# Performance work log

Measured on AMD Instinct MI355X. Metric: run time of the kernel, lower is better.

## Reference

```python
import jax, jax.numpy as jnp
import numpy as np

N_NODES = 2000
N_EDGES = 32000
B, T = 16, 20
OUT = 8      # GAT out_feats (num_heads=1)
HID = 24     # LSTM hidden
FC_OUT = 160  # num_airports * prediction_horizon = 20*8
FCC_OUT = 20
NEG_SLOPE = 0.2


def setup_inputs() -> dict:
    key = jax.random.key(0)
    ks = jax.random.split(key, 20)
    s = 0.1
    return {
        "x": jax.random.normal(ks[0], (B, T, N_NODES, 1), jnp.float32),
        "edge_w": jax.random.uniform(ks[1], (B, T, N_EDGES, 1), jnp.float32),
        "src": jax.random.randint(ks[2], (N_EDGES,), 0, N_NODES, dtype=jnp.int32),
        "dst": jax.random.randint(ks[3], (N_EDGES,), 0, N_NODES, dtype=jnp.int32),
        # EdgeGATConv params
        "W_node": jax.random.normal(ks[4], (1, OUT), jnp.float32) * s,
        "W_edge": jax.random.normal(ks[5], (1, OUT), jnp.float32) * s,
        "attn_l": jax.random.normal(ks[6], (OUT,), jnp.float32) * s,
        "attn_e": jax.random.normal(ks[7], (OUT,), jnp.float32) * s,
        "attn_r": jax.random.normal(ks[8], (OUT,), jnp.float32) * s,
        "gat_b": jnp.zeros((OUT,), jnp.float32),
        # LSTM params (PyTorch gate order i,f,g,o)
        "w_ih": jax.random.normal(ks[9], (4 * HID, OUT), jnp.float32) * s,
        "w_hh": jax.random.normal(ks[10], (4 * HID, HID), jnp.float32) * s,
        "b_ih": jnp.zeros((4 * HID,), jnp.float32),
        "b_hh": jnp.zeros((4 * HID,), jnp.float32),
        # fc / fcc
        "fc_w": jax.random.normal(ks[11], (FC_OUT, HID), jnp.float32) * s,
        "fc_b": jnp.zeros((FC_OUT,), jnp.float32),
        "fcc_w": jax.random.normal(ks[12], (FCC_OUT, 8 * 20), jnp.float32) * s,
        "fcc_b": jnp.zeros((FCC_OUT,), jnp.float32),
    }


def _gat_graph(xg, wg, src, dst, W_node, W_edge, attn_l, attn_e, attn_r, gat_b):
    # xg: [N,1], wg: [E,1] -> pooled graph feature [OUT]
    fs = xg @ W_node                      # [N,OUT] projected node feats
    fe = wg @ W_edge                      # [E,OUT] projected edge feats
    el = fs @ attn_l                      # [N]
    er = fs @ attn_r                      # [N]  (dst == src features, homogeneous graph)
    ee = fe @ attn_e                      # [E]
    e = jax.nn.leaky_relu(el[src] + ee + er[dst], NEG_SLOPE)  # [E]
    # edge_softmax over incoming edges of each dst node
    emax = jax.ops.segment_max(e, dst, num_segments=N_NODES)  # [N]
    num = jnp.exp(e - emax[dst])
    den = jax.ops.segment_sum(num, dst, num_segments=N_NODES)
    a = num / den[dst]                    # [E]
    msg = a[:, None] * (fs[src] + fe)     # [E,OUT]
    rst = jax.ops.segment_sum(msg, dst, num_segments=N_NODES) + gat_b  # [N,OUT]
    return rst.mean(axis=0)               # graph mean-pool -> [OUT]


def reference(x, edge_w, src, dst, W_node, W_edge, attn_l, attn_e, attn_r, gat_b,
              w_ih, w_hh, b_ih, b_hh, fc_w, fc_b, fcc_w, fcc_b):
    # GAT per (series, time) graph, vmapped over flattened B*T axis
    xf = x.reshape(B * T, N_NODES, 1)
    wf = edge_w.reshape(B * T, N_EDGES, 1)
    gat = jax.vmap(lambda xg, wg: _gat_graph(xg, wg, src, dst, W_node, W_edge,
                                             attn_l, attn_e, attn_r, gat_b))
    feats = gat(xf, wf).reshape(B, T, OUT)  # [B,T,8]
    # Dropout(0.1) -> identity in eval mode

    # LSTM (batch_first), zero initial state
    def step(carry, xt):
        h, c = carry
        g = xt @ w_ih.T + h @ w_hh.T + b_ih + b_hh  # [B,4H]
        i, f, gg, o = jnp.split(g, 4, axis=-1)
        c = jax.nn.sigmoid(f) * c + jax.nn.sigmoid(i) * jnp.tanh(gg)
        h = jax.nn.sigmoid(o) * jnp.tanh(c)
        return (h, c), h

    h0 = jnp.zeros((B, HID), feats.dtype)
    (_, _), hs = jax.lax.scan(step, (h0, h0), jnp.swapaxes(feats, 0, 1))
    outputs = jnp.swapaxes(hs, 0, 1)      # [B,T,24]; squeeze(0) is a no-op for B>1

    out = outputs @ fc_w.T + fc_b         # [B,T,160]
    out = out.reshape(-1, 8 * 20) @ fcc_w.T + fcc_b  # [B*T,20]
    return out
```

## Files before the change

kernel.cpp:

```cpp
#include <hip/hip_runtime.h>
#include <math.h>

#define N_NODES 2000
#define N_EDGES 32000
#define BB 16
#define TT 20
#define NG (BB*TT)
#define OUTF 8
#define HID 24
#define FC_OUTD 160
#define FCC_OUTD 20

#define SC_DEN 4194304.0f
#define SC_T1  1048576.0f
#define SC_T2  4194304.0f


__global__ __launch_bounds__(1024) void gat_fused(
    const float* __restrict__ x, const float* __restrict__ edge_w,
    const int* __restrict__ src, const int* __restrict__ dst,
    const float* __restrict__ W_node, const float* __restrict__ W_edge,
    const float* __restrict__ attn_l, const float* __restrict__ attn_e,
    const float* __restrict__ attn_r, const float* __restrict__ gat_b,
    float* __restrict__ feats)
{
    __shared__ float xs[N_NODES];
    __shared__ int   aden[N_NODES];
    __shared__ int   at1[N_NODES];
    __shared__ int   at2[N_NODES];
    __shared__ double wr1[16], wr2[16];

    const int g   = blockIdx.x;
    const int tid = threadIdx.x;

    float cl = 0.f, ce = 0.f, cr = 0.f;
#pragma unroll
    for (int k = 0; k < OUTF; ++k) {
        cl += W_node[k] * attn_l[k];
        cr += W_node[k] * attn_r[k];
        ce += W_edge[k] * attn_e[k];
    }

    const float* xg = x + (size_t)g * N_NODES;
    const float* wg = edge_w + (size_t)g * N_EDGES;

    {
        const float4* xg4 = (const float4*)xg;
        for (int i = tid; i < N_NODES/4; i += 1024)
            ((float4*)xs)[i] = xg4[i];
        for (int i = tid; i < N_NODES; i += 1024) {
            aden[i] = 0; at1[i] = 0; at2[i] = 0;
        }
    }
    __syncthreads();

    const int4*   src4 = (const int4*)src;
    const int4*   dst4 = (const int4*)dst;
    const float4* wg4  = (const float4*)wg;
#pragma unroll
    for (int k = 0; k < (N_EDGES/4 + 1023) / 1024; ++k) {
        int c = tid + k * 1024;
        if (c < N_EDGES/4) {
            int4   sv = src4[c];
            int4   dv = dst4[c];
            float4 wv = wg4[c];
#pragma unroll
            for (int j = 0; j < 4; ++j) {
                int   s = (&sv.x)[j];
                int   d = (&dv.x)[j];
                float w = (&wv.x)[j];
                float xsv = xs[s];
                float ev  = cl * xsv + ce * w + cr * xs[d];
                ev = fmaxf(ev, 0.2f * ev);
                float num = __expf(ev);
                atomicAdd(&aden[d], __float2int_rn(num * SC_DEN));
                atomicAdd(&at1[d],  __float2int_rn(num * xsv * SC_T1));
                atomicAdd(&at2[d],  __float2int_rn(num * w * SC_T2));
            }
        }
    }
    __syncthreads();

    double s1 = 0.0, s2 = 0.0;
    for (int n = tid; n < N_NODES; n += 1024) {
        int deni = aden[n];
        if (deni > 0) {
            double inv = 1.0 / (double)deni;
            s1 += (double)at1[n] * 4.0 * inv;
            s2 += (double)at2[n] * inv;
        }
    }
#pragma unroll
    for (int off = 32; off > 0; off >>= 1) {
        s1 += __shfl_down(s1, off, 64);
        s2 += __shfl_down(s2, off, 64);
    }
    int wave = tid >> 6, lane = tid & 63;
    if (lane == 0) { wr1[wave] = s1; wr2[wave] = s2; }
    __syncthreads();
    if (tid == 0) {
        double a = 0.0, c = 0.0;
#pragma unroll
        for (int w = 0; w < 16; ++w) { a += wr1[w]; c += wr2[w]; }
#pragma unroll
        for (int k = 0; k < OUTF; ++k)
            feats[g * OUTF + k] = gat_b[k] +
                (float)((a * (double)W_node[k] + c * (double)W_edge[k]) / (double)N_NODES);
    }
}


__device__ __forceinline__ float fast_sigmoid(float v) {
    return 1.f / (1.f + __expf(-v));
}
__device__ __forceinline__ float fast_tanh(float v) {
    float t = __expf(2.f * v);
    return (t - 1.f) / (t + 1.f);
}

__global__ __launch_bounds__(128) void lstm_head(
    const float* __restrict__ feats,
    const float* __restrict__ w_ih, const float* __restrict__ w_hh,
    const float* __restrict__ b_ih, const float* __restrict__ b_hh,
    const float* __restrict__ fc_w, const float* __restrict__ fc_b,
    const float* __restrict__ fcc_w, const float* __restrict__ fcc_b,
    float* __restrict__ out)
{
    __shared__ float s_fccw[FCC_OUTD * FC_OUTD];
    __shared__ float s_fcw[FC_OUTD * HID];
    __shared__ float s_fcb[FC_OUTD];
    __shared__ float s_M[FCC_OUTD * HID];
    __shared__ float s_b2[FCC_OUTD];
    __shared__ float s_xt[TT * OUTF];
    __shared__ float s_g[96];
    __shared__ float s_h[HID], s_c[HID];
    __shared__ float s_hs[TT * HID];

    const int b   = blockIdx.x;
    const int tid = threadIdx.x;

    for (int i = tid; i < FCC_OUTD * FC_OUTD; i += 128) s_fccw[i] = fcc_w[i];
    for (int i = tid; i < FC_OUTD * HID;      i += 128) s_fcw[i]  = fc_w[i];
    for (int i = tid; i < FC_OUTD;            i += 128) s_fcb[i]  = fc_b[i];
    for (int i = tid; i < TT * OUTF;          i += 128) s_xt[i]   = feats[b * TT * OUTF + i];
    if (tid < HID) { s_h[tid] = 0.f; s_c[tid] = 0.f; }

    float rw_ih[OUTF], rw_hh[HID], rbias = 0.f;
    if (tid < 96) {
        rbias = b_ih[tid] + b_hh[tid];
#pragma unroll
        for (int k = 0; k < OUTF; ++k) rw_ih[k] = w_ih[tid * OUTF + k];
#pragma unroll
        for (int k = 0; k < HID; ++k) rw_hh[k] = w_hh[tid * HID + k];
    }
    __syncthreads();

    for (int u = tid; u < FCC_OUTD * HID; u += 128) {
        int j = u / HID, h = u % HID;
        float acc = 0.f;
        for (int m = 0; m < FC_OUTD; ++m)
            acc += s_fccw[j * FC_OUTD + m] * s_fcw[m * HID + h];
        s_M[u] = acc;
    }
    if (tid < FCC_OUTD) {
        float acc = fcc_b[tid];
        for (int m = 0; m < FC_OUTD; ++m) acc += s_fccw[tid * FC_OUTD + m] * s_fcb[m];
        s_b2[tid] = acc;
    }

    for (int t = 0; t < TT; ++t) {
        if (tid < 96) {
            float acc = rbias;
            const float* xt = &s_xt[t * OUTF];
#pragma unroll
            for (int k = 0; k < OUTF; ++k) acc += xt[k] * rw_ih[k];
#pragma unroll
            for (int k = 0; k < HID; ++k) acc += s_h[k] * rw_hh[k];
            s_g[tid] = acc;
        }
        __syncthreads();
        if (tid < HID) {
            float i_ = fast_sigmoid(s_g[tid]);
            float f_ = fast_sigmoid(s_g[24 + tid]);
            float g_ = fast_tanh(s_g[48 + tid]);
            float o_ = fast_sigmoid(s_g[72 + tid]);
            float c = f_ * s_c[tid] + i_ * g_;
            s_c[tid] = c;
            float h = o_ * fast_tanh(c);
            s_h[tid] = h;
            s_hs[t * HID + tid] = h;
        }
        __syncthreads();
    }

    for (int u = tid; u < TT * FCC_OUTD; u += 128) {
        int t = u / FCC_OUTD, j = u % FCC_OUTD;
        float acc = s_b2[j];
        const float* hr = &s_hs[t * HID];
#pragma unroll
        for (int h = 0; h < HID; ++h) acc += hr[h] * s_M[j * HID + h];
        out[(b * TT + t) * FCC_OUTD + j] = acc;
    }
}

extern "C" void kernel_launch(void* const* d_in, const int* in_sizes, int n_in,
                              void* d_out, int out_size, void* d_ws, size_t ws_size,
                              hipStream_t stream) {
    const float* x      = (const float*)d_in[0];
    const float* edge_w = (const float*)d_in[1];
    const int*   src    = (const int*)d_in[2];
    const int*   dst    = (const int*)d_in[3];
    const float* W_node = (const float*)d_in[4];
    const float* W_edge = (const float*)d_in[5];
    const float* attn_l = (const float*)d_in[6];
    const float* attn_e = (const float*)d_in[7];
    const float* attn_r = (const float*)d_in[8];
    const float* gat_b  = (const float*)d_in[9];
    const float* w_ih   = (const float*)d_in[10];
    const float* w_hh   = (const float*)d_in[11];
    const float* b_ih   = (const float*)d_in[12];
    const float* b_hh   = (const float*)d_in[13];
    const float* fc_w   = (const float*)d_in[14];
    const float* fc_b   = (const float*)d_in[15];
    const float* fcc_w  = (const float*)d_in[16];
    const float* fcc_b  = (const float*)d_in[17];

    float* feats = (float*)d_ws;
    float* out   = (float*)d_out;

    gat_fused<<<NG, 1024, 0, stream>>>(x, edge_w, src, dst, W_node, W_edge,
                                       attn_l, attn_e, attn_r, gat_b, feats);
    lstm_head<<<BB, 128, 0, stream>>>(feats, w_ih, w_hh, b_ih, b_hh,
                                      fc_w, fc_b, fcc_w, fcc_b, out);
}
```

Baseline: 50.56 us.

## Precompute fcc·fc product in extra GAT block and hoist LSTM input projection

Adds an extra block to the GAT launch that computes the folded fcc_w·fc_w matrix and bias once into workspace, running alongside the graph blocks. The LSTM kernel then no longer loads the large fc weights or repeats that fold in each of its 16 blocks. It also precomputes the input-to-gate projection for all timesteps in parallel before the serial recurrence, which shortens each step. The cost is more workspace traffic and one extra block in the GAT grid.

```diff
diff --git a/kernel.cpp b/kernel.cpp
--- a/kernel.cpp
+++ b/kernel.cpp
@@ -16,13 +16,16 @@
 #define SC_T2  4194304.0f
 
 
+
 __global__ __launch_bounds__(1024) void gat_fused(
     const float* __restrict__ x, const float* __restrict__ edge_w,
     const int* __restrict__ src, const int* __restrict__ dst,
     const float* __restrict__ W_node, const float* __restrict__ W_edge,
     const float* __restrict__ attn_l, const float* __restrict__ attn_e,
     const float* __restrict__ attn_r, const float* __restrict__ gat_b,
-    float* __restrict__ feats)
+    const float* __restrict__ fc_w, const float* __restrict__ fc_b,
+    const float* __restrict__ fcc_w, const float* __restrict__ fcc_b,
+    float* __restrict__ ws)
 {
     __shared__ float xs[N_NODES];
     __shared__ int   aden[N_NODES];
@@ -30,8 +33,28 @@
     __shared__ int   at2[N_NODES];
     __shared__ double wr1[16], wr2[16];
 
-    const int g   = blockIdx.x;
     const int tid = threadIdx.x;
+
+    if (blockIdx.x == NG) {
+        if (tid < FCC_OUTD * HID) {
+            int j = tid / HID, h = tid % HID;
+            float acc = 0.f;
+#pragma unroll 4
+            for (int m = 0; m < FC_OUTD; ++m)
+                acc += fcc_w[j * FC_OUTD + m] * fc_w[m * HID + h];
+            ws[NG * OUTF + tid] = acc;
+        } else if (tid < FCC_OUTD * HID + FCC_OUTD) {
+            int j = tid - FCC_OUTD * HID;
+            float acc = fcc_b[j];
+#pragma unroll 4
+            for (int m = 0; m < FC_OUTD; ++m)
+                acc += fcc_w[j * FC_OUTD + m] * fc_b[m];
+            ws[NG * OUTF + FCC_OUTD * HID + j] = acc;
+        }
+        return;
+    }
+
+    const int g = blockIdx.x;
 
     float cl = 0.f, ce = 0.f, cr = 0.f;
 #pragma unroll
@@ -104,7 +127,7 @@
         for (int w = 0; w < 16; ++w) { a += wr1[w]; c += wr2[w]; }
 #pragma unroll
         for (int k = 0; k < OUTF; ++k)
-            feats[g * OUTF + k] = gat_b[k] +
+            ws[g * OUTF + k] = gat_b[k] +
                 (float)((a * (double)W_node[k] + c * (double)W_edge[k]) / (double)N_NODES);
     }
 }
@@ -119,19 +142,16 @@
 }
 
 __global__ __launch_bounds__(128) void lstm_head(
-    const float* __restrict__ feats,
+    const float* __restrict__ ws,
     const float* __restrict__ w_ih, const float* __restrict__ w_hh,
     const float* __restrict__ b_ih, const float* __restrict__ b_hh,
-    const float* __restrict__ fc_w, const float* __restrict__ fc_b,
-    const float* __restrict__ fcc_w, const float* __restrict__ fcc_b,
     float* __restrict__ out)
 {
-    __shared__ float s_fccw[FCC_OUTD * FC_OUTD];
-    __shared__ float s_fcw[FC_OUTD * HID];
-    __shared__ float s_fcb[FC_OUTD];
     __shared__ float s_M[FCC_OUTD * HID];
     __shared__ float s_b2[FCC_OUTD];
     __shared__ float s_xt[TT * OUTF];
+    __shared__ float s_bias[96];
+    __shared__ float s_xg[TT * 96];
     __shared__ float s_g[96];
     __shared__ float s_h[HID], s_c[HID];
     __shared__ float s_hs[TT * HID];
@@ -139,41 +159,32 @@
     const int b   = blockIdx.x;
     const int tid = threadIdx.x;
 
-    for (int i = tid; i < FCC_OUTD * FC_OUTD; i += 128) s_fccw[i] = fcc_w[i];
-    for (int i = tid; i < FC_OUTD * HID;      i += 128) s_fcw[i]  = fc_w[i];
-    for (int i = tid; i < FC_OUTD;            i += 128) s_fcb[i]  = fc_b[i];
-    for (int i = tid; i < TT * OUTF;          i += 128) s_xt[i]   = feats[b * TT * OUTF + i];
+    for (int i = tid; i < FCC_OUTD * HID; i += 128) s_M[i]  = ws[NG * OUTF + i];
+    if (tid < FCC_OUTD) s_b2[tid] = ws[NG * OUTF + FCC_OUTD * HID + tid];
+    for (int i = tid; i < TT * OUTF; i += 128) s_xt[i] = ws[b * TT * OUTF + i];
+    if (tid < 96) s_bias[tid] = b_ih[tid] + b_hh[tid];
     if (tid < HID) { s_h[tid] = 0.f; s_c[tid] = 0.f; }
 
-    float rw_ih[OUTF], rw_hh[HID], rbias = 0.f;
+    float rw_hh[HID];
     if (tid < 96) {
-        rbias = b_ih[tid] + b_hh[tid];
-#pragma unroll
-        for (int k = 0; k < OUTF; ++k) rw_ih[k] = w_ih[tid * OUTF + k];
 #pragma unroll
         for (int k = 0; k < HID; ++k) rw_hh[k] = w_hh[tid * HID + k];
     }
     __syncthreads();
 
-    for (int u = tid; u < FCC_OUTD * HID; u += 128) {
-        int j = u / HID, h = u % HID;
-        float acc = 0.f;
-        for (int m = 0; m < FC_OUTD; ++m)
-            acc += s_fccw[j * FC_OUTD + m] * s_fcw[m * HID + h];
-        s_M[u] = acc;
-    }
-    if (tid < FCC_OUTD) {
-        float acc = fcc_b[tid];
-        for (int m = 0; m < FC_OUTD; ++m) acc += s_fccw[tid * FC_OUTD + m] * s_fcb[m];
-        s_b2[tid] = acc;
-    }
+    for (int u = tid; u < TT * 96; u += 128) {
+        int t = u / 96, j = u % 96;
+        float acc = s_bias[j];
+        const float* xt = &s_xt[t * OUTF];
+#pragma unroll
+        for (int k = 0; k < OUTF; ++k) acc += xt[k] * w_ih[j * OUTF + k];
+        s_xg[u] = acc;
+    }
+    __syncthreads();
 
     for (int t = 0; t < TT; ++t) {
         if (tid < 96) {
-            float acc = rbias;
-            const float* xt = &s_xt[t * OUTF];
-#pragma unroll
-            for (int k = 0; k < OUTF; ++k) acc += xt[k] * rw_ih[k];
+            float acc = s_xg[t * 96 + tid];
 #pragma unroll
             for (int k = 0; k < HID; ++k) acc += s_h[k] * rw_hh[k];
             s_g[tid] = acc;
@@ -225,11 +236,11 @@
     const float* fcc_w  = (const float*)d_in[16];
     const float* fcc_b  = (const float*)d_in[17];
 
-    float* feats = (float*)d_ws;
-    float* out   = (float*)d_out;
-
-    gat_fused<<<NG, 1024, 0, stream>>>(x, edge_w, src, dst, W_node, W_edge,
-                                       attn_l, attn_e, attn_r, gat_b, feats);
-    lstm_head<<<BB, 128, 0, stream>>>(feats, w_ih, w_hh, b_ih, b_hh,
-                                      fc_w, fc_b, fcc_w, fcc_b, out);
-}
+    float* ws  = (float*)d_ws;
+    float* out = (float*)d_out;
+
+    gat_fused<<<NG + 1, 1024, 0, stream>>>(x, edge_w, src, dst, W_node, W_edge,
+                                           attn_l, attn_e, attn_r, gat_b,
+                                           fc_w, fc_b, fcc_w, fcc_b, ws);
+    lstm_head<<<BB, 128, 0, stream>>>(ws, w_ih, w_hh, b_ih, b_hh, out);
+}
```

Result: faster. 45.82 us (-9.4%).
